# Performance work log

Measured on AMD Instinct MI355X. Metric: run time of the kernel, lower is better.

Reference implementation:

```python
import jax, jax.numpy as jnp
import numpy as np

N_NODES = 100_000
N_HYPEREDGES = 200_000
NNZ = 2_000_000
D = 64
H = 32
KEEP_RATIO = 0.5


def setup_inputs() -> dict:
    key = jax.random.key(0)
    ks = jax.random.split(key, 5)
    x = jax.random.normal(ks[0], (N_NODES, D), jnp.float32)
    V_idx = jax.random.randint(ks[1], (NNZ,), 0, N_NODES)
    E_idx = jax.random.randint(ks[2], (NNZ,), 0, N_HYPEREDGES)
    W1 = jax.random.normal(ks[3], (2 * D, H), jnp.float32) * (1.0 / np.sqrt(2 * D))
    b1 = jnp.zeros((H,), jnp.float32)
    W2 = jax.random.normal(ks[4], (H, 1), jnp.float32) * (1.0 / np.sqrt(H))
    b2 = jnp.zeros((1,), jnp.float32)
    return dict(x=x, V_idx=V_idx, E_idx=E_idx, W1=W1, b1=b1, W2=W2, b2=b2)


def _segment_mean(vals, idx, num_segments):
    # index_add sum / clamped count, matching reduce_incidence_to_edge / index_mean
    s = jax.ops.segment_sum(vals, idx, num_segments=num_segments)
    c = jax.ops.segment_sum(jnp.ones((vals.shape[0],), vals.dtype), idx,
                            num_segments=num_segments)
    c = jnp.clip(c, 1.0, None)
    if vals.ndim == 2:
        c = c[:, None]
    return s / c


def reference(x, V_idx, E_idx, W1, b1, W2, b2):
    xv = x[V_idx]                                   # [nnz, D] gather
    edge_feats = _segment_mean(xv, E_idx, N_HYPEREDGES)  # [E, D]
    pair = jnp.concatenate([xv, edge_feats[E_idx]], axis=-1)  # [nnz, 2D]
    h = jax.nn.relu(pair @ W1 + b1)                 # [nnz, H]
    probs = jax.nn.sigmoid((h @ W2 + b2)[:, 0])     # [nnz]

    k = max(1, int(KEEP_RATIO * NNZ))
    keep_ids = jax.lax.top_k(probs, k)[1]           # is_test=True path (deterministic)
    hard = jnp.zeros_like(probs).at[keep_ids].set(1.0)
    soft = jax.lax.stop_gradient(hard - probs) + probs  # straight-through

    edge_probs = _segment_mean(jax.lax.stop_gradient(probs), E_idx, N_HYPEREDGES)
    edge_soft = _segment_mean(soft, E_idx, N_HYPEREDGES)
    edge_hard = (_segment_mean(hard, E_idx, N_HYPEREDGES) > 0).astype(jnp.float32)
    return (probs, soft, hard, edge_probs, edge_soft, edge_hard)
```

## Files before the change

### kernel.cpp

```cpp
#include <hip/hip_runtime.h>
#include <math.h>

#define N_NODES   100000
#define N_EDGES   200000
#define NNZ       2000000
#define K_KEEP    1000000
#define BANDCAP   131072
#define TIECAP    4096
#define DELTA     1.0e-4f
#define SCAN_BLOCKS 196
#define USCALE (4294967296.0 / 4.0e-3)

#define SC_PASSES 8
#define SC_EPP    (N_EDGES / SC_PASSES)
#define SC_BLOCKS 2048

#define OFF_PAB   ((size_t)0)
#define OFF_PB32  ((size_t)25600000)
#define OFF_VJ    ((size_t)33600000)
#define OFF_RANK  ((size_t)49600000)
#define OFF_EOFF  ((size_t)57600000)
#define OFF_CUR   ((size_t)58400000)
#define OFF_BS    ((size_t)59200000)
#define OFF_BANDP ((size_t)59201024)
#define OFF_BANDJ ((size_t)59725312)
#define OFF_BANDE ((size_t)60249600)
#define OFF_BANDV ((size_t)60773888)
#define OFF_BANDK ((size_t)61298176)
#define OFF_TIEK  ((size_t)62346752)
#define OFF_TIEJ  ((size_t)62379520)
#define OFF_TIEP  ((size_t)62395904)
#define OFF_FLAG  ((size_t)62412288)
#define OFF_ECNT  ((size_t)64412288)
#define OFF_HIST  ((size_t)65212288)
#define OFF_ST    ((size_t)65245056)
#define ZERO_OFF  OFF_FLAG
#define ZERO_LEN  ((size_t)(65245312 - 62412288))

struct SelState {
    unsigned int B1;
    unsigned int rem1;
    float lo_edge, hi_edge;
    unsigned int bB1;
    unsigned int brem1;
    unsigned int bU0;
    unsigned int brem2;
    unsigned int _pad0[8];
    unsigned int n_hi;      unsigned int _pad1[15];
    unsigned int band_n;    unsigned int _pad2[15];
    unsigned int tie_n;     unsigned int _pad3[15];
};

__device__ __forceinline__ unsigned int band_u32(double key, float lo) {
    double t = (key - (double)lo) * USCALE;
    t = t < 0.0 ? 0.0 : (t > 4294967295.0 ? 4294967295.0 : t);
    return (unsigned int)t;
}

__global__ void proj_kernel(const float* __restrict__ x, const float* __restrict__ W1,
                            float2* __restrict__ p_ab2) {
    __shared__ float sW[128 * 32];
    __shared__ float sx[8][64];
    for (int t = threadIdx.x; t < 128 * 32; t += 256) sW[t] = W1[t];
    int base = blockIdx.x * 8;
    for (int t = threadIdx.x; t < 512; t += 256) {
        int n = t >> 6, d = t & 63;
        int g = base + n;
        sx[n][d] = (g < N_NODES) ? x[(size_t)g * 64 + d] : 0.f;
    }
    __syncthreads();
    int ln = threadIdx.x >> 5;
    int k  = threadIdx.x & 31;
    int node = base + ln;
    if (node >= N_NODES) return;
    float sa = 0.f, sb = 0.f;
    for (int d = 0; d < 64; ++d) {
        float xv = sx[ln][d];
        sa += xv * sW[d * 32 + k];
        sb += xv * sW[(64 + d) * 32 + k];
    }
    p_ab2[(size_t)node * 32 + k] = make_float2(sa, sb);
}

__global__ void count_rank_kernel(const int* __restrict__ E, unsigned int* __restrict__ edge_cnt,
                                  unsigned int* __restrict__ rank) {
    unsigned int base = blockIdx.x * 2048 + threadIdx.x;
    int ev[8];
    unsigned int rr[8];
    #pragma unroll
    for (int c = 0; c < 8; ++c) {
        unsigned int j = base + 256u * c;
        if (j < NNZ) ev[c] = E[j];
    }
    #pragma unroll
    for (int c = 0; c < 8; ++c) {
        unsigned int j = base + 256u * c;
        if (j < NNZ) rr[c] = atomicAdd(&edge_cnt[ev[c]], 1u);
    }
    #pragma unroll
    for (int c = 0; c < 8; ++c) {
        unsigned int j = base + 256u * c;
        if (j < NNZ) rank[j] = rr[c];
    }
}

__global__ void scanA_kernel(const unsigned int* __restrict__ edge_cnt,
                             unsigned int* __restrict__ edge_off, unsigned int* __restrict__ bsums) {
    __shared__ unsigned int s[256];
    int tid = threadIdx.x;
    int base = blockIdx.x * 1024 + tid * 4;
    unsigned int v0 = (base + 0 < N_EDGES) ? edge_cnt[base + 0] : 0u;
    unsigned int v1 = (base + 1 < N_EDGES) ? edge_cnt[base + 1] : 0u;
    unsigned int v2 = (base + 2 < N_EDGES) ? edge_cnt[base + 2] : 0u;
    unsigned int v3 = (base + 3 < N_EDGES) ? edge_cnt[base + 3] : 0u;
    unsigned int tsum = v0 + v1 + v2 + v3;
    s[tid] = tsum;
    __syncthreads();
    for (int off = 1; off < 256; off <<= 1) {
        unsigned int t = (tid >= off) ? s[tid - off] : 0u;
        __syncthreads();
        s[tid] += t;
        __syncthreads();
    }
    unsigned int excl = s[tid] - tsum;
    if (base + 0 < N_EDGES) edge_off[base + 0] = excl;
    if (base + 1 < N_EDGES) edge_off[base + 1] = excl + v0;
    if (base + 2 < N_EDGES) edge_off[base + 2] = excl + v0 + v1;
    if (base + 3 < N_EDGES) edge_off[base + 3] = excl + v0 + v1 + v2;
    if (tid == 255) bsums[blockIdx.x] = s[255];
}

__global__ void scanB_kernel(unsigned int* __restrict__ bsums) {
    __shared__ unsigned int s[256];
    int tid = threadIdx.x;
    unsigned int v = (tid < SCAN_BLOCKS) ? bsums[tid] : 0u;
    s[tid] = v;
    __syncthreads();
    for (int off = 1; off < 256; off <<= 1) {
        unsigned int t = (tid >= off) ? s[tid - off] : 0u;
        __syncthreads();
        s[tid] += t;
        __syncthreads();
    }
    if (tid < SCAN_BLOCKS) bsums[tid] = s[tid] - v;
}

__global__ void scanC_kernel(unsigned int* __restrict__ edge_off, const unsigned int* __restrict__ bsums) {
    int i = blockIdx.x * 256 + threadIdx.x;
    if (i >= N_EDGES) return;
    edge_off[i] = edge_off[i] + bsums[i >> 10];
}

__global__ void scatter_kernel(const int* __restrict__ V, const int* __restrict__ E,
                               const unsigned int* __restrict__ edge_off,
                               const unsigned int* __restrict__ rank,
                               uint2* __restrict__ vj) {
    unsigned int pass = blockIdx.x & 7u;
    unsigned int q    = blockIdx.x >> 3;
    unsigned int elo  = pass * SC_EPP;
    const unsigned int stride = (SC_BLOCKS / 8) * 256;
    for (unsigned int j = q * 256u + threadIdx.x; j < NNZ; j += stride) {
        unsigned int e = (unsigned int)__builtin_nontemporal_load(E + j);
        if (e - elo < (unsigned int)SC_EPP) {
            unsigned int pp = edge_off[e] + __builtin_nontemporal_load(rank + j);
            unsigned int v  = (unsigned int)__builtin_nontemporal_load(V + j);
            vj[pp] = make_uint2(v, j);
        }
    }
}

__global__ void edge_logit_kernel(const uint2* __restrict__ vj,
                                  const unsigned int* __restrict__ edge_off,
                                  const unsigned int* __restrict__ edge_cnt,
                                  const float2* __restrict__ p_ab2,
                                  const float* __restrict__ b1, const float* __restrict__ W2,
                                  const float* __restrict__ b2,
                                  float* __restrict__ probs_b, float* __restrict__ o_ep) {
    __shared__ float slog[4][32];
    __shared__ unsigned int sv[4][32];
    int e = blockIdx.x * 4 + (threadIdx.x >> 6);
    if (e >= N_EDGES) return;
    int w    = threadIdx.x >> 6;
    int lane = threadIdx.x & 63;
    int g    = lane >> 4;
    int l    = lane & 15;

    unsigned int off = edge_off[e];
    unsigned int deg = edge_cnt[e];
    unsigned int mind = deg < 32u ? deg : 32u;

    if ((unsigned int)lane < mind) sv[w][lane] = vj[off + lane].x;

    float2 w2  = ((const float2*)W2)[l];
    float2 bb1 = ((const float2*)b1)[l];
    float  b2v = b2[0];

    float2 aA[8];
    float2 bacc = make_float2(0.f, 0.f);
    #pragma unroll 8
    for (unsigned int m = 0; m < 8u; ++m) {
        if (4u * m >= mind) break;
        unsigned int idx = 4u * m + (unsigned int)g;
        if (idx < mind) {
            unsigned int v = sv[w][idx];
            float4 r = reinterpret_cast<const float4*>(p_ab2 + (size_t)v * 32u)[l];
            aA[m] = make_float2(r.x, r.z);
            bacc.x += r.y;
            bacc.y += r.w;
        } else {
            aA[m] = make_float2(0.f, 0.f);
        }
    }
    for (unsigned int ii = 32u + (unsigned int)g; ii < deg; ii += 4u) {
        unsigned int v = vj[off + ii].x;
        float4 r = reinterpret_cast<const float4*>(p_ab2 + (size_t)v * 32u)[l];
        bacc.x += r.y;
        bacc.y += r.w;
    }
    bacc.x += __shfl_xor(bacc.x, 16);
    bacc.y += __shfl_xor(bacc.y, 16);
    bacc.x += __shfl_xor(bacc.x, 32);
    bacc.y += __shfl_xor(bacc.y, 32);
    float cc = (float)(deg > 1u ? deg : 1u);
    float2 em2 = make_float2(bacc.x / cc + bb1.x, bacc.y / cc + bb1.y);

    #pragma unroll 8
    for (unsigned int m = 0; m < 8u; ++m) {
        if (4u * m >= mind) break;
        unsigned int idx = 4u * m + (unsigned int)g;
        float h0 = aA[m].x + em2.x;
        float h1 = aA[m].y + em2.y;
        h0 = h0 > 0.f ? h0 : 0.f;
        h1 = h1 > 0.f ? h1 : 0.f;
        float t = h0 * w2.x + h1 * w2.y;
        #pragma unroll
        for (int o = 8; o > 0; o >>= 1) t += __shfl_down(t, o, 16);
        if (l == 0 && idx < mind) slog[w][idx] = t;
    }
    float prsum = 0.f;
    if ((unsigned int)lane < mind) {
        float pr = 1.f / (1.f + __expf(-(slog[w][lane] + b2v)));
        probs_b[off + lane] = pr;
        prsum = pr;
    }
    for (unsigned int ii = 32u + (unsigned int)g; ii < deg; ii += 4u) {
        unsigned int v = vj[off + ii].x;
        float4 r = reinterpret_cast<const float4*>(p_ab2 + (size_t)v * 32u)[l];
        float h0 = r.x + em2.x;
        float h1 = r.z + em2.y;
        h0 = h0 > 0.f ? h0 : 0.f;
        h1 = h1 > 0.f ? h1 : 0.f;
        float t = h0 * w2.x + h1 * w2.y;
        #pragma unroll
        for (int o = 8; o > 0; o >>= 1) t += __shfl_down(t, o, 16);
        if (l == 0) {
            float pr = 1.f / (1.f + __expf(-(t + b2v)));
            probs_b[off + ii] = pr;
            prsum += pr;
        }
    }
    #pragma unroll
    for (int o = 32; o > 0; o >>= 1) prsum += __shfl_down(prsum, o, 64);
    if (lane == 0) o_ep[e] = prsum / cc;
}

__device__ __forceinline__ void radix_sel_256(const unsigned int* __restrict__ h,
                                              unsigned int target,
                                              unsigned int* csum, unsigned int* sres,
                                              unsigned int& out_bin, unsigned int& out_rem) {
    int t = threadIdx.x;
    unsigned int b[8];
    unsigned int s = 0;
    #pragma unroll
    for (int i = 0; i < 8; ++i) { b[i] = h[t * 8 + i]; s += b[i]; }
    csum[t] = s;
    __syncthreads();
    for (int off = 1; off < 256; off <<= 1) {
        unsigned int v = (t + off < 256) ? csum[t + off] : 0u;
        __syncthreads();
        csum[t] += v;
        __syncthreads();
    }
    unsigned int above = csum[t] - s;
    if (above < target && target <= above + s) {
        unsigned int rem = target - above;
        unsigned int cum = 0;
        #pragma unroll
        for (int i = 7; i >= 0; --i) {
            if (rem <= cum + b[i]) {
                sres[0] = (unsigned int)(t * 8 + i);
                sres[1] = rem - cum;
                break;
            }
            cum += b[i];
        }
    }
    __syncthreads();
    out_bin = sres[0];
    out_rem = sres[1];
    __syncthreads();
}

__global__ void hist1_kernel(const float* __restrict__ probs_b, unsigned int* __restrict__ hist) {
    __shared__ unsigned int lh[4][2048 + 8];
    for (int t = threadIdx.x; t < 4 * (2048 + 8); t += 256) ((unsigned int*)lh)[t] = 0;
    __syncthreads();
    int sub = threadIdx.x & 3;
    const float4* p4 = (const float4*)probs_b;
    for (unsigned int i = blockIdx.x * 256 + threadIdx.x; i < NNZ / 4; i += gridDim.x * 256) {
        float4 v = p4[i];
        atomicAdd(&lh[sub][__float_as_uint(v.x) >> 21], 1u);
        atomicAdd(&lh[sub][__float_as_uint(v.y) >> 21], 1u);
        atomicAdd(&lh[sub][__float_as_uint(v.z) >> 21], 1u);
        atomicAdd(&lh[sub][__float_as_uint(v.w) >> 21], 1u);
    }
    __syncthreads();
    for (int t = threadIdx.x; t < 2048; t += 256) {
        unsigned int s = lh[0][t] + lh[1][t] + lh[2][t] + lh[3][t];
        if (s) atomicAdd(&hist[t], s);
    }
}

__global__ void hist2_kernel(const float* __restrict__ probs_b,
                             const unsigned int* __restrict__ hist_ro,
                             unsigned int* __restrict__ hist) {
    __shared__ unsigned int csum[256];
    __shared__ unsigned int sres[2];
    __shared__ unsigned int lh[2048];
    unsigned int B1, rem_unused;
    radix_sel_256(hist_ro, (unsigned int)K_KEEP, csum, sres, B1, rem_unused);
    for (int t = threadIdx.x; t < 2048; t += 256) lh[t] = 0;
    __syncthreads();
    for (unsigned int i = blockIdx.x * 256 + threadIdx.x; i < NNZ; i += gridDim.x * 256) {
        unsigned int key = __float_as_uint(probs_b[i]);
        if ((key >> 21) == B1) atomicAdd(&lh[(key >> 10) & 2047u], 1u);
    }
    __syncthreads();
    for (int t = threadIdx.x; t < 2048; t += 256)
        if (lh[t]) atomicAdd(&hist[2048 + t], lh[t]);
}

__global__ void bandsel_kernel(const float* __restrict__ probs_b, const int* __restrict__ E,
                               const uint2* __restrict__ vj,
                               const unsigned int* __restrict__ hist,
                               SelState* __restrict__ st,
                               unsigned int* __restrict__ band_p, unsigned int* __restrict__ band_j,
                               unsigned int* __restrict__ band_e, unsigned int* __restrict__ band_v) {
    __shared__ unsigned int csum[256];
    __shared__ unsigned int sres[2];
    __shared__ unsigned int whi[4], wband[4];
    __shared__ unsigned int sbase, scur;
    unsigned int B1, rem1, bin2, rem2_unused;
    radix_sel_256(hist, (unsigned int)K_KEEP, csum, sres, B1, rem1);
    radix_sel_256(hist + 2048, rem1, csum, sres, bin2, rem2_unused);
    unsigned int P = (B1 << 21) | (bin2 << 10);
    float lo = __uint_as_float(P) - DELTA;
    float hi = __uint_as_float(P + 1024u) + DELTA;
    if (threadIdx.x == 0) { st->lo_edge = lo; st->hi_edge = hi; }
    unsigned int nhi = 0, nband = 0;
    for (unsigned int p = blockIdx.x * 256 + threadIdx.x; p < NNZ; p += gridDim.x * 256) {
        float pk = probs_b[p];
        if (pk > hi) nhi++;
        else if (pk >= lo) nband++;
    }
    #pragma unroll
    for (int o = 32; o > 0; o >>= 1) {
        nhi   += __shfl_down(nhi, o);
        nband += __shfl_down(nband, o);
    }
    if ((threadIdx.x & 63) == 0) { whi[threadIdx.x >> 6] = nhi; wband[threadIdx.x >> 6] = nband; }
    __syncthreads();
    if (threadIdx.x == 0) {
        unsigned int th = whi[0] + whi[1] + whi[2] + whi[3];
        unsigned int tb = wband[0] + wband[1] + wband[2] + wband[3];
        if (th) atomicAdd(&st->n_hi, th);
        sbase = tb ? atomicAdd(&st->band_n, tb) : 0u;
        scur = 0;
    }
    __syncthreads();
    for (unsigned int p = blockIdx.x * 256 + threadIdx.x; p < NNZ; p += gridDim.x * 256) {
        float pk = probs_b[p];
        if (pk <= hi && pk >= lo) {
            unsigned int s = sbase + atomicAdd(&scur, 1u);
            if (s < BANDCAP) {
                uint2 t = vj[p];
                band_p[s] = p;
                band_j[s] = t.y;
                band_e[s] = (unsigned int)E[t.y];
                band_v[s] = t.x;
            }
        }
    }
}

__global__ void rescue_kernel(const uint2* __restrict__ vj,
                              const unsigned int* __restrict__ edge_off,
                              const unsigned int* __restrict__ edge_cnt,
                              const float* __restrict__ x, const float* __restrict__ W1,
                              const float* __restrict__ b1, const float* __restrict__ W2,
                              const float* __restrict__ b2,
                              const unsigned int* __restrict__ band_e,
                              const unsigned int* __restrict__ band_v,
                              const SelState* __restrict__ st,
                              unsigned long long* __restrict__ band_key) {
    unsigned int n = st->band_n; if (n > BANDCAP) n = BANDCAP;
    if (blockIdx.x * 8 >= n) return;
    __shared__ float sW[128 * 32];
    for (int t = threadIdx.x; t < 128 * 32; t += 256) sW[t] = W1[t];
    __syncthreads();
    unsigned int g = blockIdx.x * 8 + (threadIdx.x >> 5);
    if (g >= n) return;
    int k = threadIdx.x & 31;
    unsigned int v = band_v[g];
    unsigned int e = band_e[g];
    unsigned int off = edge_off[e];
    unsigned int deg = edge_cnt[e];

    const float* xv = x + (size_t)v * 64u;
    double a = 0.0;
    #pragma unroll 8
    for (int d = 0; d < 64; ++d) a += (double)xv[d] * (double)sW[d * 32 + k];
    double bsum = 0.0;
    for (unsigned int m = off; m < off + deg; ++m) {
        const float* xm = x + (size_t)vj[m].x * 64u;
        double acc = 0.0;
        #pragma unroll 8
        for (int d = 0; d < 64; ++d) acc += (double)xm[d] * (double)sW[(64 + d) * 32 + k];
        bsum += acc;
    }
    double cc = (double)(deg > 1u ? deg : 1u);
    double h = a + bsum / cc + (double)b1[k];
    h = h > 0.0 ? h : 0.0;
    double t = h * (double)W2[k];
    #pragma unroll
    for (int o = 16; o > 0; o >>= 1) t += __shfl_down(t, o, 32);
    if (k == 0) {
        double pr = 1.0 / (1.0 + exp(-(t + (double)b2[0])));
        band_key[g] = (unsigned long long)__double_as_longlong(pr);
    }
}

__global__ void bhist1_kernel(const unsigned long long* __restrict__ band_key,
                              const SelState* __restrict__ st, unsigned int* __restrict__ hist) {
    __shared__ unsigned int lh[2048];
    for (int t = threadIdx.x; t < 2048; t += 256) lh[t] = 0;
    __syncthreads();
    unsigned int n = st->band_n; if (n > BANDCAP) n = BANDCAP;
    float lo = st->lo_edge;
    for (unsigned int i = blockIdx.x * 256 + threadIdx.x; i < n; i += gridDim.x * 256) {
        unsigned int u = band_u32(__longlong_as_double((long long)band_key[i]), lo);
        atomicAdd(&lh[u >> 21], 1u);
    }
    __syncthreads();
    for (int t = threadIdx.x; t < 2048; t += 256)
        if (lh[t]) atomicAdd(&hist[4096 + t], lh[t]);
}

__global__ void bhist2_kernel(const unsigned long long* __restrict__ band_key,
                              const SelState* __restrict__ st, unsigned int* __restrict__ hist) {
    __shared__ unsigned int csum[256];
    __shared__ unsigned int sres[2];
    __shared__ unsigned int lh[2048];
    unsigned int bB1, rem_unused;
    radix_sel_256(hist + 4096, (unsigned int)K_KEEP - st->n_hi, csum, sres, bB1, rem_unused);
    for (int t = threadIdx.x; t < 2048; t += 256) lh[t] = 0;
    __syncthreads();
    unsigned int n = st->band_n; if (n > BANDCAP) n = BANDCAP;
    float lo = st->lo_edge;
    for (unsigned int i = blockIdx.x * 256 + threadIdx.x; i < n; i += gridDim.x * 256) {
        unsigned int u = band_u32(__longlong_as_double((long long)band_key[i]), lo);
        if ((u >> 21) == bB1) atomicAdd(&lh[(u >> 10) & 2047u], 1u);
    }
    __syncthreads();
    for (int t = threadIdx.x; t < 2048; t += 256)
        if (lh[t]) atomicAdd(&hist[6144 + t], lh[t]);
}

__global__ void btie_kernel(const unsigned long long* __restrict__ band_key,
                            const unsigned int* __restrict__ band_j,
                            const unsigned int* __restrict__ band_p,
                            const unsigned int* __restrict__ hist,
                            SelState* __restrict__ st, unsigned char* __restrict__ flag,
                            unsigned long long* __restrict__ tie_k,
                            unsigned int* __restrict__ tie_j, unsigned int* __restrict__ tie_p) {
    __shared__ unsigned int csum[256];
    __shared__ unsigned int sres[2];
    unsigned int bB1, brem1, bin2, brem2;
    radix_sel_256(hist + 4096, (unsigned int)K_KEEP - st->n_hi, csum, sres, bB1, brem1);
    radix_sel_256(hist + 6144, brem1, csum, sres, bin2, brem2);
    unsigned int U0 = (bB1 << 21) | (bin2 << 10);
    if (threadIdx.x == 0) { st->bU0 = U0; st->brem2 = brem2; }
    unsigned int n = st->band_n; if (n > BANDCAP) n = BANDCAP;
    unsigned int i = blockIdx.x * 256 + threadIdx.x;
    if (i >= n) return;
    float lo = st->lo_edge;
    unsigned long long key = band_key[i];
    unsigned int u = band_u32(__longlong_as_double((long long)key), lo);
    if (u >= U0 + 1024u) {
        flag[band_p[i]] = 2u;
    } else if (u >= U0) {
        unsigned int s = atomicAdd(&st->tie_n, 1u);
        if (s < TIECAP) { tie_k[s] = key; tie_j[s] = band_j[i]; tie_p[s] = band_p[i]; }
    }
}

__global__ void btierank_kernel(const unsigned long long* __restrict__ tie_k,
                                const unsigned int* __restrict__ tie_j,
                                const unsigned int* __restrict__ tie_p,
                                const SelState* __restrict__ st, unsigned char* __restrict__ flag) {
    unsigned int n = st->tie_n; if (n > TIECAP) n = TIECAP;
    unsigned int need = st->brem2;
    for (unsigned int i = threadIdx.x; i < n; i += 256) {
        unsigned long long ki = tie_k[i];
        unsigned int ji = tie_j[i];
        unsigned int r = 0;
        for (unsigned int q = 0; q < n; ++q) {
            unsigned long long kq = tie_k[q];
            if (kq > ki || (kq == ki && tie_j[q] < ji)) r++;
        }
        if (r < need) flag[tie_p[i]] = 2u;
    }
}

__global__ void out_kernel(const float* __restrict__ probs_b, const unsigned char* __restrict__ flag,
                           const int* __restrict__ E, const unsigned int* __restrict__ rank,
                           const unsigned int* __restrict__ edge_off, const SelState* __restrict__ st,
                           float* __restrict__ o_probs, float* __restrict__ o_soft, float* __restrict__ o_hard) {
    unsigned int j0 = (blockIdx.x * 256 + threadIdx.x) * 4u;
    if (j0 >= NNZ) return;
    float hi = st->hi_edge;
    int4  e4 = *reinterpret_cast<const int4*>(E + j0);
    uint4 r4 = *reinterpret_cast<const uint4*>(rank + j0);
    unsigned int p0 = edge_off[e4.x] + r4.x;
    unsigned int p1 = edge_off[e4.y] + r4.y;
    unsigned int p2 = edge_off[e4.z] + r4.z;
    unsigned int p3 = edge_off[e4.w] + r4.w;
    float pk0 = probs_b[p0], pk1 = probs_b[p1], pk2 = probs_b[p2], pk3 = probs_b[p3];
    unsigned char f0 = flag[p0], f1 = flag[p1], f2 = flag[p2], f3 = flag[p3];
    float4 pr = make_float4(pk0, pk1, pk2, pk3);
    float4 hb = make_float4((pk0 > hi || f0 == 2u) ? 1.f : 0.f,
                            (pk1 > hi || f1 == 2u) ? 1.f : 0.f,
                            (pk2 > hi || f2 == 2u) ? 1.f : 0.f,
                            (pk3 > hi || f3 == 2u) ? 1.f : 0.f);
    *reinterpret_cast<float4*>(o_probs + j0) = pr;
    *reinterpret_cast<float4*>(o_soft  + j0) = hb;
    *reinterpret_cast<float4*>(o_hard  + j0) = hb;
}

__global__ void edge_out_kernel(const float* __restrict__ probs_b, const unsigned char* __restrict__ flag,
                                const unsigned int* __restrict__ edge_off,
                                const unsigned int* __restrict__ edge_cnt,
                                const SelState* __restrict__ st,
                                float* __restrict__ o_es, float* __restrict__ o_eh) {
    unsigned int e = blockIdx.x * 256 + threadIdx.x;
    if (e >= N_EDGES) return;
    float hi = st->hi_edge;
    unsigned int off = edge_off[e], deg = edge_cnt[e];
    unsigned int cnt = 0;
    for (unsigned int i = 0; i < deg; ++i)
        cnt += (probs_b[off + i] > hi || flag[off + i] == 2u) ? 1u : 0u;
    float cc = (float)(deg > 1u ? deg : 1u);
    o_es[e] = (float)cnt / cc;
    o_eh[e] = cnt ? 1.f : 0.f;
}

extern "C" void kernel_launch(void* const* d_in, const int* in_sizes, int n_in,
                              void* d_out, int out_size, void* d_ws, size_t ws_size,
                              hipStream_t stream) {
    const float* x  = (const float*)d_in[0];
    const int*   V  = (const int*)d_in[1];
    const int*   E  = (const int*)d_in[2];
    const float* W1 = (const float*)d_in[3];
    const float* b1 = (const float*)d_in[4];
    const float* W2 = (const float*)d_in[5];
    const float* b2 = (const float*)d_in[6];

    float* out     = (float*)d_out;
    float* o_probs = out;
    float* o_soft  = out + NNZ;
    float* o_hard  = out + 2 * (size_t)NNZ;
    float* o_ep    = out + 3 * (size_t)NNZ;
    float* o_es    = out + 3 * (size_t)NNZ + N_EDGES;
    float* o_eh    = out + 3 * (size_t)NNZ + 2 * (size_t)N_EDGES;

    char* w = (char*)d_ws;
    float2*             p_ab2    = (float2*)(w + OFF_PAB);
    float*              probs_b  = (float*)(w + OFF_PB32);
    uint2*              vj       = (uint2*)(w + OFF_VJ);
    unsigned int*       rank     = (unsigned int*)(w + OFF_RANK);
    unsigned int*       edge_off = (unsigned int*)(w + OFF_EOFF);
    unsigned int*       bsums    = (unsigned int*)(w + OFF_BS);
    unsigned int*       band_p   = (unsigned int*)(w + OFF_BANDP);
    unsigned int*       band_j   = (unsigned int*)(w + OFF_BANDJ);
    unsigned int*       band_e   = (unsigned int*)(w + OFF_BANDE);
    unsigned int*       band_v   = (unsigned int*)(w + OFF_BANDV);
    unsigned long long* band_key = (unsigned long long*)(w + OFF_BANDK);
    unsigned long long* tie_k    = (unsigned long long*)(w + OFF_TIEK);
    unsigned int*       tie_j    = (unsigned int*)(w + OFF_TIEJ);
    unsigned int*       tie_p    = (unsigned int*)(w + OFF_TIEP);
    unsigned char*      flag     = (unsigned char*)(w + OFF_FLAG);
    unsigned int*       edge_cnt = (unsigned int*)(w + OFF_ECNT);
    unsigned int*       hist     = (unsigned int*)(w + OFF_HIST);
    SelState*           st       = (SelState*)(w + OFF_ST);

    hipMemsetAsync(w + ZERO_OFF, 0, ZERO_LEN, stream);

    proj_kernel<<<(N_NODES + 7) / 8, 256, 0, stream>>>(x, W1, p_ab2);

    count_rank_kernel<<<(NNZ + 2047) / 2048, 256, 0, stream>>>(E, edge_cnt, rank);
    scanA_kernel<<<SCAN_BLOCKS, 256, 0, stream>>>(edge_cnt, edge_off, bsums);
    scanB_kernel<<<1, 256, 0, stream>>>(bsums);
    scanC_kernel<<<(N_EDGES + 255) / 256, 256, 0, stream>>>(edge_off, bsums);
    scatter_kernel<<<SC_BLOCKS, 256, 0, stream>>>(V, E, edge_off, rank, vj);

    edge_logit_kernel<<<(N_EDGES + 3) / 4, 256, 0, stream>>>(vj, edge_off, edge_cnt,
                                                             p_ab2, b1, W2, b2, probs_b, o_ep);

    hist1_kernel<<<1024, 256, 0, stream>>>(probs_b, hist);
    hist2_kernel<<<1024, 256, 0, stream>>>(probs_b, hist, hist);
    bandsel_kernel<<<1024, 256, 0, stream>>>(probs_b, E, vj, hist, st,
                                             band_p, band_j, band_e, band_v);
    rescue_kernel<<<BANDCAP / 8, 256, 0, stream>>>(vj, edge_off, edge_cnt, x, W1, b1, W2, b2,
                                                   band_e, band_v, st, band_key);

    bhist1_kernel<<<64, 256, 0, stream>>>(band_key, st, hist);
    bhist2_kernel<<<64, 256, 0, stream>>>(band_key, st, hist);
    btie_kernel<<<BANDCAP / 256, 256, 0, stream>>>(band_key, band_j, band_p, hist, st, flag,
                                                   tie_k, tie_j, tie_p);
    btierank_kernel<<<1, 256, 0, stream>>>(tie_k, tie_j, tie_p, st, flag);

    out_kernel<<<(NNZ / 4 + 255) / 256, 256, 0, stream>>>(probs_b, flag, E, rank, edge_off, st,
                                                          o_probs, o_soft, o_hard);
    edge_out_kernel<<<(N_EDGES + 255) / 256, 256, 0, stream>>>(probs_b, flag, edge_off, edge_cnt, st,
                                                               o_es, o_eh);
}
```

Before: 556.7 us.

## Merge independent kernels and drop small scan and histogram launches

```diff
diff --git a/kernel.cpp b/kernel.cpp
--- a/kernel.cpp
+++ b/kernel.cpp
@@ -14,6 +14,11 @@
 #define SC_PASSES 8
 #define SC_EPP    (N_EDGES / SC_PASSES)
 #define SC_BLOCKS 2048
+
+#define CNT_BLOCKS  ((NNZ + 2047) / 2048)
+#define PROJ_BLOCKS ((N_NODES + 63) / 64)
+#define OUT_BLOCKS  ((NNZ / 4 + 255) / 256)
+#define EOUT_BLOCKS ((N_EDGES + 255) / 256)
 
 #define OFF_PAB   ((size_t)0)
 #define OFF_PB32  ((size_t)25600000)
@@ -57,50 +62,56 @@
     return (unsigned int)t;
 }
 
-__global__ void proj_kernel(const float* __restrict__ x, const float* __restrict__ W1,
-                            float2* __restrict__ p_ab2) {
+__global__ void proj_count_kernel(const float* __restrict__ x, const float* __restrict__ W1,
+                                  float2* __restrict__ p_ab2,
+                                  const int* __restrict__ E, unsigned int* __restrict__ edge_cnt,
+                                  unsigned int* __restrict__ rank) {
     __shared__ float sW[128 * 32];
     __shared__ float sx[8][64];
+    if (blockIdx.x < CNT_BLOCKS) {
+        unsigned int base = blockIdx.x * 2048 + threadIdx.x;
+        int ev[8];
+        unsigned int rr[8];
+        #pragma unroll
+        for (int c = 0; c < 8; ++c) {
+            unsigned int j = base + 256u * c;
+            if (j < NNZ) ev[c] = E[j];
+        }
+        #pragma unroll
+        for (int c = 0; c < 8; ++c) {
+            unsigned int j = base + 256u * c;
+            if (j < NNZ) rr[c] = atomicAdd(&edge_cnt[ev[c]], 1u);
+        }
+        #pragma unroll
+        for (int c = 0; c < 8; ++c) {
+            unsigned int j = base + 256u * c;
+            if (j < NNZ) rank[j] = rr[c];
+        }
+        return;
+    }
+    int pb = blockIdx.x - CNT_BLOCKS;
     for (int t = threadIdx.x; t < 128 * 32; t += 256) sW[t] = W1[t];
-    int base = blockIdx.x * 8;
-    for (int t = threadIdx.x; t < 512; t += 256) {
-        int n = t >> 6, d = t & 63;
-        int g = base + n;
-        sx[n][d] = (g < N_NODES) ? x[(size_t)g * 64 + d] : 0.f;
-    }
-    __syncthreads();
     int ln = threadIdx.x >> 5;
     int k  = threadIdx.x & 31;
-    int node = base + ln;
-    if (node >= N_NODES) return;
-    float sa = 0.f, sb = 0.f;
-    for (int d = 0; d < 64; ++d) {
-        float xv = sx[ln][d];
-        sa += xv * sW[d * 32 + k];
-        sb += xv * sW[(64 + d) * 32 + k];
-    }
-    p_ab2[(size_t)node * 32 + k] = make_float2(sa, sb);
-}
-
-__global__ void count_rank_kernel(const int* __restrict__ E, unsigned int* __restrict__ edge_cnt,
-                                  unsigned int* __restrict__ rank) {
-    unsigned int base = blockIdx.x * 2048 + threadIdx.x;
-    int ev[8];
-    unsigned int rr[8];
-    #pragma unroll
-    for (int c = 0; c < 8; ++c) {
-        unsigned int j = base + 256u * c;
-        if (j < NNZ) ev[c] = E[j];
-    }
-    #pragma unroll
-    for (int c = 0; c < 8; ++c) {
-        unsigned int j = base + 256u * c;
-        if (j < NNZ) rr[c] = atomicAdd(&edge_cnt[ev[c]], 1u);
-    }
-    #pragma unroll
-    for (int c = 0; c < 8; ++c) {
-        unsigned int j = base + 256u * c;
-        if (j < NNZ) rank[j] = rr[c];
+    for (int g = 0; g < 8; ++g) {
+        int base = pb * 64 + g * 8;
+        __syncthreads();
+        for (int t = threadIdx.x; t < 512; t += 256) {
+            int n = t >> 6, d = t & 63;
+            int gn = base + n;
+            sx[n][d] = (gn < N_NODES) ? x[(size_t)gn * 64 + d] : 0.f;
+        }
+        __syncthreads();
+        int node = base + ln;
+        if (node < N_NODES) {
+            float sa = 0.f, sb = 0.f;
+            for (int d = 0; d < 64; ++d) {
+                float xv = sx[ln][d];
+                sa += xv * sW[d * 32 + k];
+                sb += xv * sW[(64 + d) * 32 + k];
+            }
+            p_ab2[(size_t)node * 32 + k] = make_float2(sa, sb);
+        }
     }
 }
 
@@ -130,25 +141,17 @@
     if (tid == 255) bsums[blockIdx.x] = s[255];
 }
 
-__global__ void scanB_kernel(unsigned int* __restrict__ bsums) {
-    __shared__ unsigned int s[256];
-    int tid = threadIdx.x;
-    unsigned int v = (tid < SCAN_BLOCKS) ? bsums[tid] : 0u;
-    s[tid] = v;
-    __syncthreads();
-    for (int off = 1; off < 256; off <<= 1) {
-        unsigned int t = (tid >= off) ? s[tid - off] : 0u;
-        __syncthreads();
-        s[tid] += t;
-        __syncthreads();
-    }
-    if (tid < SCAN_BLOCKS) bsums[tid] = s[tid] - v;
-}
-
 __global__ void scanC_kernel(unsigned int* __restrict__ edge_off, const unsigned int* __restrict__ bsums) {
+    __shared__ unsigned int sred[4];
+    unsigned int need = blockIdx.x >> 2;
+    unsigned int v = (threadIdx.x < need) ? bsums[threadIdx.x] : 0u;
+    #pragma unroll
+    for (int o = 32; o > 0; o >>= 1) v += __shfl_down(v, o);
+    if ((threadIdx.x & 63) == 0) sred[threadIdx.x >> 6] = v;
+    __syncthreads();
+    unsigned int base = sred[0] + sred[1] + sred[2] + sred[3];
     int i = blockIdx.x * 256 + threadIdx.x;
-    if (i >= N_EDGES) return;
-    edge_off[i] = edge_off[i] + bsums[i >> 10];
+    if (i < N_EDGES) edge_off[i] += base;
 }
 
 __global__ void scatter_kernel(const int* __restrict__ V, const int* __restrict__ E,
@@ -331,9 +334,15 @@
     radix_sel_256(hist_ro, (unsigned int)K_KEEP, csum, sres, B1, rem_unused);
     for (int t = threadIdx.x; t < 2048; t += 256) lh[t] = 0;
     __syncthreads();
-    for (unsigned int i = blockIdx.x * 256 + threadIdx.x; i < NNZ; i += gridDim.x * 256) {
-        unsigned int key = __float_as_uint(probs_b[i]);
-        if ((key >> 21) == B1) atomicAdd(&lh[(key >> 10) & 2047u], 1u);
+    const float4* p4 = (const float4*)probs_b;
+    for (unsigned int i = blockIdx.x * 256 + threadIdx.x; i < NNZ / 4; i += gridDim.x * 256) {
+        float4 v = p4[i];
+        unsigned int kx = __float_as_uint(v.x), ky = __float_as_uint(v.y);
+        unsigned int kz = __float_as_uint(v.z), kw = __float_as_uint(v.w);
+        if ((kx >> 21) == B1) atomicAdd(&lh[(kx >> 10) & 2047u], 1u);
+        if ((ky >> 21) == B1) atomicAdd(&lh[(ky >> 10) & 2047u], 1u);
+        if ((kz >> 21) == B1) atomicAdd(&lh[(kz >> 10) & 2047u], 1u);
+        if ((kw >> 21) == B1) atomicAdd(&lh[(kw >> 10) & 2047u], 1u);
     }
     __syncthreads();
     for (int t = threadIdx.x; t < 2048; t += 256)
@@ -348,8 +357,7 @@
                                unsigned int* __restrict__ band_e, unsigned int* __restrict__ band_v) {
     __shared__ unsigned int csum[256];
     __shared__ unsigned int sres[2];
-    __shared__ unsigned int whi[4], wband[4];
-    __shared__ unsigned int sbase, scur;
+    __shared__ unsigned int whi[4];
     unsigned int B1, rem1, bin2, rem2_unused;
     radix_sel_256(hist, (unsigned int)K_KEEP, csum, sres, B1, rem1);
     radix_sel_256(hist + 2048, rem1, csum, sres, bin2, rem2_unused);
@@ -357,31 +365,12 @@
     float lo = __uint_as_float(P) - DELTA;
     float hi = __uint_as_float(P + 1024u) + DELTA;
     if (threadIdx.x == 0) { st->lo_edge = lo; st->hi_edge = hi; }
-    unsigned int nhi = 0, nband = 0;
+    unsigned int nhi = 0;
     for (unsigned int p = blockIdx.x * 256 + threadIdx.x; p < NNZ; p += gridDim.x * 256) {
         float pk = probs_b[p];
         if (pk > hi) nhi++;
-        else if (pk >= lo) nband++;
-    }
-    #pragma unroll
-    for (int o = 32; o > 0; o >>= 1) {
-        nhi   += __shfl_down(nhi, o);
-        nband += __shfl_down(nband, o);
-    }
-    if ((threadIdx.x & 63) == 0) { whi[threadIdx.x >> 6] = nhi; wband[threadIdx.x >> 6] = nband; }
-    __syncthreads();
-    if (threadIdx.x == 0) {
-        unsigned int th = whi[0] + whi[1] + whi[2] + whi[3];
-        unsigned int tb = wband[0] + wband[1] + wband[2] + wband[3];
-        if (th) atomicAdd(&st->n_hi, th);
-        sbase = tb ? atomicAdd(&st->band_n, tb) : 0u;
-        scur = 0;
-    }
-    __syncthreads();
-    for (unsigned int p = blockIdx.x * 256 + threadIdx.x; p < NNZ; p += gridDim.x * 256) {
-        float pk = probs_b[p];
-        if (pk <= hi && pk >= lo) {
-            unsigned int s = sbase + atomicAdd(&scur, 1u);
+        else if (pk >= lo) {
+            unsigned int s = atomicAdd(&st->band_n, 1u);
             if (s < BANDCAP) {
                 uint2 t = vj[p];
                 band_p[s] = p;
@@ -390,6 +379,14 @@
                 band_v[s] = t.x;
             }
         }
+    }
+    #pragma unroll
+    for (int o = 32; o > 0; o >>= 1) nhi += __shfl_down(nhi, o);
+    if ((threadIdx.x & 63) == 0) whi[threadIdx.x >> 6] = nhi;
+    __syncthreads();
+    if (threadIdx.x == 0) {
+        unsigned int th = whi[0] + whi[1] + whi[2] + whi[3];
+        if (th) atomicAdd(&st->n_hi, th);
     }
 }
 
@@ -402,7 +399,8 @@
                               const unsigned int* __restrict__ band_e,
                               const unsigned int* __restrict__ band_v,
                               const SelState* __restrict__ st,
-                              unsigned long long* __restrict__ band_key) {
+                              unsigned long long* __restrict__ band_key,
+                              unsigned int* __restrict__ hist) {
     unsigned int n = st->band_n; if (n > BANDCAP) n = BANDCAP;
     if (blockIdx.x * 8 >= n) return;
     __shared__ float sW[128 * 32];
@@ -437,23 +435,9 @@
     if (k == 0) {
         double pr = 1.0 / (1.0 + exp(-(t + (double)b2[0])));
         band_key[g] = (unsigned long long)__double_as_longlong(pr);
-    }
-}
-
-__global__ void bhist1_kernel(const unsigned long long* __restrict__ band_key,
-                              const SelState* __restrict__ st, unsigned int* __restrict__ hist) {
-    __shared__ unsigned int lh[2048];
-    for (int t = threadIdx.x; t < 2048; t += 256) lh[t] = 0;
-    __syncthreads();
-    unsigned int n = st->band_n; if (n > BANDCAP) n = BANDCAP;
-    float lo = st->lo_edge;
-    for (unsigned int i = blockIdx.x * 256 + threadIdx.x; i < n; i += gridDim.x * 256) {
-        unsigned int u = band_u32(__longlong_as_double((long long)band_key[i]), lo);
-        atomicAdd(&lh[u >> 21], 1u);
-    }
-    __syncthreads();
-    for (int t = threadIdx.x; t < 2048; t += 256)
-        if (lh[t]) atomicAdd(&hist[4096 + t], lh[t]);
+        unsigned int u = band_u32(pr, st->lo_edge);
+        atomicAdd(&hist[4096 + (u >> 21)], 1u);
+    }
 }
 
 __global__ void bhist2_kernel(const unsigned long long* __restrict__ band_key,
@@ -483,14 +467,15 @@
                             SelState* __restrict__ st, unsigned char* __restrict__ flag,
                             unsigned long long* __restrict__ tie_k,
                             unsigned int* __restrict__ tie_j, unsigned int* __restrict__ tie_p) {
+    unsigned int n = st->band_n; if (n > BANDCAP) n = BANDCAP;
+    if (blockIdx.x != 0 && blockIdx.x * 256u >= n) return;
     __shared__ unsigned int csum[256];
     __shared__ unsigned int sres[2];
     unsigned int bB1, brem1, bin2, brem2;
     radix_sel_256(hist + 4096, (unsigned int)K_KEEP - st->n_hi, csum, sres, bB1, brem1);
     radix_sel_256(hist + 6144, brem1, csum, sres, bin2, brem2);
     unsigned int U0 = (bB1 << 21) | (bin2 << 10);
-    if (threadIdx.x == 0) { st->bU0 = U0; st->brem2 = brem2; }
-    unsigned int n = st->band_n; if (n > BANDCAP) n = BANDCAP;
+    if (blockIdx.x == 0 && threadIdx.x == 0) { st->bU0 = U0; st->brem2 = brem2; }
     unsigned int i = blockIdx.x * 256 + threadIdx.x;
     if (i >= n) return;
     float lo = st->lo_edge;
@@ -522,46 +507,45 @@
     }
 }
 
-__global__ void out_kernel(const float* __restrict__ probs_b, const unsigned char* __restrict__ flag,
-                           const int* __restrict__ E, const unsigned int* __restrict__ rank,
-                           const unsigned int* __restrict__ edge_off, const SelState* __restrict__ st,
-                           float* __restrict__ o_probs, float* __restrict__ o_soft, float* __restrict__ o_hard) {
-    unsigned int j0 = (blockIdx.x * 256 + threadIdx.x) * 4u;
-    if (j0 >= NNZ) return;
+__global__ void outs_kernel(const float* __restrict__ probs_b, const unsigned char* __restrict__ flag,
+                            const int* __restrict__ E, const unsigned int* __restrict__ rank,
+                            const unsigned int* __restrict__ edge_off,
+                            const unsigned int* __restrict__ edge_cnt,
+                            const SelState* __restrict__ st,
+                            float* __restrict__ o_probs, float* __restrict__ o_soft,
+                            float* __restrict__ o_hard,
+                            float* __restrict__ o_es, float* __restrict__ o_eh) {
     float hi = st->hi_edge;
-    int4  e4 = *reinterpret_cast<const int4*>(E + j0);
-    uint4 r4 = *reinterpret_cast<const uint4*>(rank + j0);
-    unsigned int p0 = edge_off[e4.x] + r4.x;
-    unsigned int p1 = edge_off[e4.y] + r4.y;
-    unsigned int p2 = edge_off[e4.z] + r4.z;
-    unsigned int p3 = edge_off[e4.w] + r4.w;
-    float pk0 = probs_b[p0], pk1 = probs_b[p1], pk2 = probs_b[p2], pk3 = probs_b[p3];
-    unsigned char f0 = flag[p0], f1 = flag[p1], f2 = flag[p2], f3 = flag[p3];
-    float4 pr = make_float4(pk0, pk1, pk2, pk3);
-    float4 hb = make_float4((pk0 > hi || f0 == 2u) ? 1.f : 0.f,
-                            (pk1 > hi || f1 == 2u) ? 1.f : 0.f,
-                            (pk2 > hi || f2 == 2u) ? 1.f : 0.f,
-                            (pk3 > hi || f3 == 2u) ? 1.f : 0.f);
-    *reinterpret_cast<float4*>(o_probs + j0) = pr;
-    *reinterpret_cast<float4*>(o_soft  + j0) = hb;
-    *reinterpret_cast<float4*>(o_hard  + j0) = hb;
-}
-
-__global__ void edge_out_kernel(const float* __restrict__ probs_b, const unsigned char* __restrict__ flag,
-                                const unsigned int* __restrict__ edge_off,
-                                const unsigned int* __restrict__ edge_cnt,
-                                const SelState* __restrict__ st,
-                                float* __restrict__ o_es, float* __restrict__ o_eh) {
-    unsigned int e = blockIdx.x * 256 + threadIdx.x;
-    if (e >= N_EDGES) return;
-    float hi = st->hi_edge;
-    unsigned int off = edge_off[e], deg = edge_cnt[e];
-    unsigned int cnt = 0;
-    for (unsigned int i = 0; i < deg; ++i)
-        cnt += (probs_b[off + i] > hi || flag[off + i] == 2u) ? 1u : 0u;
-    float cc = (float)(deg > 1u ? deg : 1u);
-    o_es[e] = (float)cnt / cc;
-    o_eh[e] = cnt ? 1.f : 0.f;
+    if (blockIdx.x < OUT_BLOCKS) {
+        unsigned int j0 = (blockIdx.x * 256 + threadIdx.x) * 4u;
+        if (j0 >= NNZ) return;
+        int4  e4 = *reinterpret_cast<const int4*>(E + j0);
+        uint4 r4 = *reinterpret_cast<const uint4*>(rank + j0);
+        unsigned int p0 = edge_off[e4.x] + r4.x;
+        unsigned int p1 = edge_off[e4.y] + r4.y;
+        unsigned int p2 = edge_off[e4.z] + r4.z;
+        unsigned int p3 = edge_off[e4.w] + r4.w;
+        float pk0 = probs_b[p0], pk1 = probs_b[p1], pk2 = probs_b[p2], pk3 = probs_b[p3];
+        unsigned char f0 = flag[p0], f1 = flag[p1], f2 = flag[p2], f3 = flag[p3];
+        float4 pr = make_float4(pk0, pk1, pk2, pk3);
+        float4 hb = make_float4((pk0 > hi || f0 == 2u) ? 1.f : 0.f,
+                                (pk1 > hi || f1 == 2u) ? 1.f : 0.f,
+                                (pk2 > hi || f2 == 2u) ? 1.f : 0.f,
+                                (pk3 > hi || f3 == 2u) ? 1.f : 0.f);
+        *reinterpret_cast<float4*>(o_probs + j0) = pr;
+        *reinterpret_cast<float4*>(o_soft  + j0) = hb;
+        *reinterpret_cast<float4*>(o_hard  + j0) = hb;
+    } else {
+        unsigned int e = (blockIdx.x - OUT_BLOCKS) * 256 + threadIdx.x;
+        if (e >= N_EDGES) return;
+        unsigned int off = edge_off[e], deg = edge_cnt[e];
+        unsigned int cnt = 0;
+        for (unsigned int i = 0; i < deg; ++i)
+            cnt += (probs_b[off + i] > hi || flag[off + i] == 2u) ? 1u : 0u;
+        float cc = (float)(deg > 1u ? deg : 1u);
+        o_es[e] = (float)cnt / cc;
+        o_eh[e] = cnt ? 1.f : 0.f;
+    }
 }
 
 extern "C" void kernel_launch(void* const* d_in, const int* in_sizes, int n_in,
@@ -605,11 +589,8 @@
 
     hipMemsetAsync(w + ZERO_OFF, 0, ZERO_LEN, stream);
 
-    proj_kernel<<<(N_NODES + 7) / 8, 256, 0, stream>>>(x, W1, p_ab2);
-
-    count_rank_kernel<<<(NNZ + 2047) / 2048, 256, 0, stream>>>(E, edge_cnt, rank);
+    proj_count_kernel<<<CNT_BLOCKS + PROJ_BLOCKS, 256, 0, stream>>>(x, W1, p_ab2, E, edge_cnt, rank);
     scanA_kernel<<<SCAN_BLOCKS, 256, 0, stream>>>(edge_cnt, edge_off, bsums);
-    scanB_kernel<<<1, 256, 0, stream>>>(bsums);
     scanC_kernel<<<(N_EDGES + 255) / 256, 256, 0, stream>>>(edge_off, bsums);
     scatter_kernel<<<SC_BLOCKS, 256, 0, stream>>>(V, E, edge_off, rank, vj);
 
@@ -621,16 +602,14 @@
     bandsel_kernel<<<1024, 256, 0, stream>>>(probs_b, E, vj, hist, st,
                                              band_p, band_j, band_e, band_v);
     rescue_kernel<<<BANDCAP / 8, 256, 0, stream>>>(vj, edge_off, edge_cnt, x, W1, b1, W2, b2,
-                                                   band_e, band_v, st, band_key);
-
-    bhist1_kernel<<<64, 256, 0, stream>>>(band_key, st, hist);
+                                                   band_e, band_v, st, band_key, hist);
+
     bhist2_kernel<<<64, 256, 0, stream>>>(band_key, st, hist);
     btie_kernel<<<BANDCAP / 256, 256, 0, stream>>>(band_key, band_j, band_p, hist, st, flag,
                                                    tie_k, tie_j, tie_p);
     btierank_kernel<<<1, 256, 0, stream>>>(tie_k, tie_j, tie_p, st, flag);
 
-    out_kernel<<<(NNZ / 4 + 255) / 256, 256, 0, stream>>>(probs_b, flag, E, rank, edge_off, st,
-                                                          o_probs, o_soft, o_hard);
-    edge_out_kernel<<<(N_EDGES + 255) / 256, 256, 0, stream>>>(probs_b, flag, edge_off, edge_cnt, st,
-                                                               o_es, o_eh);
-}
+    outs_kernel<<<OUT_BLOCKS + EOUT_BLOCKS, 256, 0, stream>>>(probs_b, flag, E, rank, edge_off,
+                                                              edge_cnt, st, o_probs, o_soft, o_hard,
+                                                              o_es, o_eh);
+}
```

After: 559.4 us. Within noise of the previous version (+0.5%).
